# Optimization experiments

Hardware: AMD Instinct MI355X
Metric: run time of the kernel (lower is better)

## Reference

```python
import jax, jax.numpy as jnp
import numpy as np

B, NQ, NC, D, H = 4, 4096, 4096, 1024, 16
HD = D // H
LN_EPS = 1e-5


def _layernorm(x, g, b):
    mu = jnp.mean(x, axis=-1, keepdims=True)
    var = jnp.var(x, axis=-1, keepdims=True)
    return (x - mu) * jax.lax.rsqrt(var + LN_EPS) * g + b


def _kernel(x):
    # elu(x) + 1  (strictly positive feature map)
    return jax.nn.elu(x) + 1.0


def setup_inputs() -> dict:
    key = jax.random.key(0)
    ks = jax.random.split(key, 12)
    s = 1.0 / np.sqrt(D)
    return {
        "query": jax.random.normal(ks[0], (B, NQ, D), jnp.float32),
        "context": jax.random.normal(ks[1], (B, NC, D), jnp.float32),
        "q_w": jax.random.uniform(ks[2], (D, D), jnp.float32, -s, s),
        "q_b": jnp.zeros((D,), jnp.float32),
        "k_w": jax.random.uniform(ks[3], (D, D), jnp.float32, -s, s),
        "k_b": jnp.zeros((D,), jnp.float32),
        "v_w": jax.random.uniform(ks[4], (D, D), jnp.float32, -s, s),
        "v_b": jnp.zeros((D,), jnp.float32),
        "o_w": jax.random.uniform(ks[5], (D, D), jnp.float32, -s, s),
        "o_b": jnp.zeros((D,), jnp.float32),
        "lnq_g": jnp.ones((D,), jnp.float32),
        "lnq_b": jnp.zeros((D,), jnp.float32),
        "lnkv_g": jnp.ones((D,), jnp.float32),
        "lnkv_b": jnp.zeros((D,), jnp.float32),
    }


def reference(query, context, q_w, q_b, k_w, k_b, v_w, v_b, o_w, o_b,
              lnq_g, lnq_b, lnkv_g, lnkv_b):
    residual = query
    q = _layernorm(query, lnq_g, lnq_b)
    c = _layernorm(context, lnkv_g, lnkv_b)

    # torch Linear: y = x @ W.T + b ; reshape to (B, H, N, Hd)
    Q = (q @ q_w.T + q_b).reshape(B, NQ, H, HD).transpose(0, 2, 1, 3)
    K = (c @ k_w.T + k_b).reshape(B, NC, H, HD).transpose(0, 2, 1, 3)
    V = (c @ v_w.T + v_b).reshape(B, NC, H, HD).transpose(0, 2, 1, 3)

    Q = _kernel(Q)
    K = _kernel(K)

    # KV: (B, H, Hd, Hd) outer-product accumulation over context length
    KV = jnp.einsum("bhnd,bhne->bhde", K, V)
    K_sum = K.sum(axis=2)                              # (B, H, Hd)
    Z = jnp.einsum("bhqd,bhd->bhq", Q, K_sum)          # (B, H, Nq)
    Z = jnp.maximum(Z, 1e-6)

    out = jnp.einsum("bhqd,bhde->bhqe", Q, KV) / Z[..., None]
    out = out.transpose(0, 2, 1, 3).reshape(B, NQ, D)
    return residual + (out @ o_w.T + o_b)
```

## Files before the change

### kernel.cpp

```cpp
#include <hip/hip_runtime.h>

#define DEV __device__ __forceinline__

typedef __attribute__((ext_vector_type(8))) short short8;
typedef __attribute__((ext_vector_type(4))) short short4v;
typedef __attribute__((ext_vector_type(4))) float f32x4;

DEV float bf2f(unsigned short u) { return __uint_as_float(((unsigned int)u) << 16); }
DEV unsigned short f2bf(float f) {
    unsigned int u = __float_as_uint(f);
    u += 0x7FFFu + ((u >> 16) & 1u);
    return (unsigned short)(u >> 16);
}

DEV float elu1(float v) { return v > 0.0f ? v + 1.0f : __expf(v); }

DEV void gload_lds16(const void* g, void* l) {
    __builtin_amdgcn_global_load_lds(
        (__attribute__((address_space(1))) unsigned int*)(g),
        (__attribute__((address_space(3))) unsigned int*)(l),
        16, 0, 0);
}

#define NROW 16384
#define DDIM 1024

__global__ __launch_bounds__(256) void ln_kernel(
    const float* __restrict__ query, const float* __restrict__ context,
    const float* __restrict__ lnq_g, const float* __restrict__ lnq_b,
    const float* __restrict__ lnk_g, const float* __restrict__ lnk_b,
    unsigned short* __restrict__ qln, unsigned short* __restrict__ cln)
{
    const int row = blockIdx.x;
    const bool isq = row < NROW;
    const int r = isq ? row : row - NROW;
    const float* src = (isq ? query : context) + (size_t)r * DDIM;
    const float* g   = isq ? lnq_g : lnk_g;
    const float* bb  = isq ? lnq_b : lnk_b;
    unsigned short* dst = (isq ? qln : cln) + (size_t)r * DDIM;

    const int tid = threadIdx.x;
    f32x4 x = *(const f32x4*)(src + tid * 4);
    float s  = x[0] + x[1] + x[2] + x[3];
    float sq = x[0]*x[0] + x[1]*x[1] + x[2]*x[2] + x[3]*x[3];
#pragma unroll
    for (int off = 32; off; off >>= 1) {
        s  += __shfl_xor(s, off);
        sq += __shfl_xor(sq, off);
    }
    __shared__ float red[8];
    const int lane = tid & 63, w = tid >> 6;
    if (lane == 0) { red[w] = s; red[4 + w] = sq; }
    __syncthreads();
    s  = red[0] + red[1] + red[2] + red[3];
    sq = red[4] + red[5] + red[6] + red[7];
    const float mu  = s * (1.0f / DDIM);
    const float var = sq * (1.0f / DDIM) - mu * mu;
    const float rstd = rsqrtf(var + 1e-5f);

    f32x4 gv = *(const f32x4*)(g + tid * 4);
    f32x4 bv = *(const f32x4*)(bb + tid * 4);
    short4v o;
#pragma unroll
    for (int j = 0; j < 4; ++j)
        o[j] = (short)f2bf((x[j] - mu) * rstd * gv[j] + bv[j]);
    *(short4v*)(dst + tid * 4) = o;
}

__global__ __launch_bounds__(256) void conv_w(
    const float* __restrict__ a, const float* __restrict__ b,
    const float* __restrict__ c, const float* __restrict__ d,
    unsigned short* __restrict__ out)
{
    const int i = blockIdx.x * 256 + threadIdx.x;
    const int mat = i >> 18;
    const int idx = (i & 262143) * 4;
    const float* src = mat == 0 ? a : mat == 1 ? b : mat == 2 ? c : d;
    f32x4 v = *(const f32x4*)(src + idx);
    short4v o;
#pragma unroll
    for (int j = 0; j < 4; ++j) o[j] = (short)f2bf(v[j]);
    *(short4v*)(out + (size_t)mat * 1048576 + idx) = o;
}

template <typename EPI>
DEV void gemm128(unsigned short* __restrict__ sA,
                 unsigned short* __restrict__ sB,
                 const unsigned short* __restrict__ Ap,
                 const unsigned short* __restrict__ Bp,
                 int m0, int n0, EPI epi)
{
    const int tid = threadIdx.x;
    const int lane = tid & 63, w = tid >> 6;
    const int wr = w >> 1, wc = w & 1;
    const int lr = lane & 15, lg = lane >> 4;

    const int srow = tid >> 3;
    const int cswz = (tid & 7) ^ (srow & 7);
    const unsigned short* gA0 = Ap + (size_t)(m0 + srow) * 1024 + cswz * 8;
    const unsigned short* gB0 = Bp + (size_t)(n0 + srow) * 1024 + cswz * 8;
    unsigned short* dA = sA + tid * 8;
    unsigned short* dB = sB + tid * 8;

    const int sw0 = ((0 + lg) ^ (lr & 7)) * 8;
    const int sw1 = ((4 + lg) ^ (lr & 7)) * 8;

    f32x4 acc[4][4];
#pragma unroll
    for (int i = 0; i < 4; ++i)
#pragma unroll
        for (int j = 0; j < 4; ++j)
#pragma unroll
            for (int e = 0; e < 4; ++e) acc[i][j][e] = 0.0f;

#define STG8(T)                                                               \
    {                                                                         \
        const int ko = (T) * 64;                                              \
        _Pragma("unroll")                                                     \
        for (int j = 0; j < 4; ++j) {                                         \
            gload_lds16(gA0 + ko + (size_t)j * 32768, dA + j * 2048);         \
            gload_lds16(gB0 + ko + (size_t)j * 32768, dB + j * 2048);         \
        }                                                                     \
    }

    STG8(0);
    for (int t = 0; t < 16; ++t) {
        asm volatile("s_waitcnt vmcnt(0)" ::: "memory");
        __builtin_amdgcn_s_barrier();

        short8 af[4], bf[4];
#pragma unroll
        for (int mt = 0; mt < 4; ++mt)
            af[mt] = *(const short8*)&sA[(wr * 64 + mt * 16 + lr) * 64 + sw0];
#pragma unroll
        for (int nt = 0; nt < 4; ++nt)
            bf[nt] = *(const short8*)&sB[(wc * 64 + nt * 16 + lr) * 64 + sw0];
        __builtin_amdgcn_s_setprio(1);
#pragma unroll
        for (int mt = 0; mt < 4; ++mt)
#pragma unroll
            for (int nt = 0; nt < 4; ++nt)
                acc[mt][nt] = __builtin_amdgcn_mfma_f32_16x16x32_bf16(
                    af[mt], bf[nt], acc[mt][nt], 0, 0, 0);
        __builtin_amdgcn_s_setprio(0);

#pragma unroll
        for (int mt = 0; mt < 4; ++mt)
            af[mt] = *(const short8*)&sA[(wr * 64 + mt * 16 + lr) * 64 + sw1];
#pragma unroll
        for (int nt = 0; nt < 4; ++nt)
            bf[nt] = *(const short8*)&sB[(wc * 64 + nt * 16 + lr) * 64 + sw1];
        asm volatile("s_waitcnt lgkmcnt(0)" ::: "memory");
        __builtin_amdgcn_s_barrier();
        if (t < 15) STG8(t + 1);
        __builtin_amdgcn_s_setprio(1);
#pragma unroll
        for (int mt = 0; mt < 4; ++mt)
#pragma unroll
            for (int nt = 0; nt < 4; ++nt)
                acc[mt][nt] = __builtin_amdgcn_mfma_f32_16x16x32_bf16(
                    af[mt], bf[nt], acc[mt][nt], 0, 0, 0);
        __builtin_amdgcn_s_setprio(0);
    }
#undef STG8

#pragma unroll
    for (int mt = 0; mt < 4; ++mt)
#pragma unroll
        for (int nt = 0; nt < 4; ++nt) {
            const int col = n0 + wc * 64 + nt * 16 + lr;
#pragma unroll
            for (int i = 0; i < 4; ++i) {
                const int row = m0 + wr * 64 + mt * 16 + lg * 4 + i;
                epi(row, col, acc[mt][nt][i]);
            }
        }
}

__global__ __launch_bounds__(256, 4) void gemm_qkv(
    const unsigned short* __restrict__ QLN, const unsigned short* __restrict__ WQ,
    const unsigned short* __restrict__ CLN, const unsigned short* __restrict__ WKV,
    unsigned short* __restrict__ Qm, unsigned short* __restrict__ KVT,
    const float* __restrict__ q_b, const float* __restrict__ k_b,
    const float* __restrict__ v_b)
{
    __shared__ __attribute__((aligned(16))) unsigned short sA[128 * 64];
    __shared__ __attribute__((aligned(16))) unsigned short sB[128 * 64];

    const int bid = blockIdx.x;
    const int l = (bid & 7) * 384 + (bid >> 3);

    if (l < 1024) {
        const int m0 = (l >> 3) * 128, n0 = (l & 7) * 128;
        gemm128(sA, sB, QLN, WQ, m0, n0,
            [&](int row, int col, float v) {
                v = elu1(v + q_b[col]);
                Qm[(size_t)row * 1024 + col] = f2bf(v);
            });
    } else {
        const int r = l - 1024;
        const int m0 = (r & 15) * 128, n0 = (r >> 4) * 128;
        gemm128(sA, sB, WKV, CLN, m0, n0,
            [&](int row, int col, float v) {
                if (row < 1024) v = elu1(v + k_b[row]);
                else            v = v + v_b[row - 1024];
                KVT[(size_t)row * NROW + col] = f2bf(v);
            });
    }
}

__global__ __launch_bounds__(256, 4) void gemm_out(
    const unsigned short* __restrict__ A2, const unsigned short* __restrict__ WO,
    float* __restrict__ Out, const float* __restrict__ o_b,
    const float* __restrict__ resid)
{
    __shared__ __attribute__((aligned(16))) unsigned short sA[128 * 64];
    __shared__ __attribute__((aligned(16))) unsigned short sB[128 * 64];

    const int bid = blockIdx.x;
    const int l = (bid & 7) * 128 + (bid >> 3);
    const int m0 = (l >> 3) * 128, n0 = (l & 7) * 128;
    gemm128(sA, sB, A2, WO, m0, n0,
        [&](int row, int col, float v) {
            Out[(size_t)row * 1024 + col] =
                v + o_b[col] + resid[(size_t)row * 1024 + col];
        });
}

__global__ __launch_bounds__(256) void kv_kernel(
    const unsigned short* __restrict__ VT, const unsigned short* __restrict__ KT,
    float* __restrict__ KVTp, float* __restrict__ Ksump)
{
    const int bh = blockIdx.x, sp = blockIdx.y;
    const int b = bh >> 4, h = bh & 15;
    const int tid = threadIdx.x, lane = tid & 63, w = tid >> 6;
    const int lr = lane & 15, lg = lane >> 4;

    f32x4 acc[4][4];
#pragma unroll
    for (int i = 0; i < 4; ++i)
#pragma unroll
        for (int j = 0; j < 4; ++j)
#pragma unroll
            for (int e = 0; e < 4; ++e) acc[i][j][e] = 0.0f;
    float kp[4] = {0.0f, 0.0f, 0.0f, 0.0f};

    const size_t colbase = (size_t)b * 4096 + sp * 1024 + w * 256 + lg * 8;
    const unsigned short* va = VT + (size_t)(h * 64 + lr) * NROW + colbase;
    const unsigned short* ka = KT + (size_t)(h * 64 + lr) * NROW + colbase;

    for (int ks = 0; ks < 8; ++ks) {
        short8 af[4], bfv[4];
#pragma unroll
        for (int mt = 0; mt < 4; ++mt)
            af[mt] = *(const short8*)(va + (size_t)mt * 16 * NROW + ks * 32);
#pragma unroll
        for (int nt = 0; nt < 4; ++nt)
            bfv[nt] = *(const short8*)(ka + (size_t)nt * 16 * NROW + ks * 32);
#pragma unroll
        for (int mt = 0; mt < 4; ++mt)
#pragma unroll
            for (int nt = 0; nt < 4; ++nt)
                acc[mt][nt] = __builtin_amdgcn_mfma_f32_16x16x32_bf16(
                    af[mt], bfv[nt], acc[mt][nt], 0, 0, 0);
#pragma unroll
        for (int nt = 0; nt < 4; ++nt)
#pragma unroll
            for (int j = 0; j < 8; ++j)
                kp[nt] += bf2f((unsigned short)bfv[nt][j]);
    }

#pragma unroll
    for (int nt = 0; nt < 4; ++nt) {
        kp[nt] += __shfl_xor(kp[nt], 16);
        kp[nt] += __shfl_xor(kp[nt], 32);
    }
    __shared__ float kred[4][64];
    if (lane < 16) {
#pragma unroll
        for (int nt = 0; nt < 4; ++nt) kred[w][nt * 16 + lane] = kp[nt];
    }

    __shared__ float red4[4][4096];
#pragma unroll
    for (int mt = 0; mt < 4; ++mt)
#pragma unroll
        for (int nt = 0; nt < 4; ++nt)
#pragma unroll
            for (int i = 0; i < 4; ++i)
                red4[w][(mt * 16 + lg * 4 + i) * 64 + nt * 16 + lr] = acc[mt][nt][i];
    __syncthreads();
    float* out = KVTp + ((size_t)sp * 64 + bh) * 4096;
    for (int i = tid; i < 4096; i += 256)
        out[i] = red4[0][i] + red4[1][i] + red4[2][i] + red4[3][i];
    if (tid < 64)
        Ksump[((size_t)sp * 64 + bh) * 64 + tid] =
            kred[0][tid] + kred[1][tid] + kred[2][tid] + kred[3][tid];
}

__global__ __launch_bounds__(256) void z_kernel(
    const unsigned short* __restrict__ Q, const float* __restrict__ Ksump,
    float* __restrict__ invZ)
{
    const int gid = blockIdx.x * 256 + threadIdx.x;
    const int n = gid >> 4, h = gid & 15;
    const int b = n >> 12;
    const unsigned short* q = Q + (size_t)n * DDIM + h * 64;
    const float* k0 = Ksump + ((size_t)((b << 4) + h)) * 64;
    float z = 0.0f;
#pragma unroll
    for (int it = 0; it < 8; ++it) {
        short8 v = *(const short8*)(q + it * 8);
#pragma unroll
        for (int j = 0; j < 8; ++j) {
            const int d = it * 8 + j;
            const float ksv = k0[d] + k0[d + 4096] + k0[d + 8192] + k0[d + 12288];
            z += bf2f((unsigned short)v[j]) * ksv;
        }
    }
    invZ[gid] = 1.0f / fmaxf(z, 1e-6f);
}

__global__ __launch_bounds__(256) void a2_kernel(
    const unsigned short* __restrict__ Q, const float* __restrict__ KVTp,
    const float* __restrict__ invZ, unsigned short* __restrict__ A2)
{
    const int m0 = blockIdx.x * 128, h = blockIdx.y;
    const int b = m0 >> 12, bh = (b << 4) + h;
    const int tid = threadIdx.x, lane = tid & 63, w = tid >> 6;
    const int wr = w >> 1, wc = w & 1;
    const int lr = lane & 15, lg = lane >> 4;

    f32x4 acc[4][2];
#pragma unroll
    for (int i = 0; i < 4; ++i)
#pragma unroll
        for (int j = 0; j < 2; ++j)
#pragma unroll
            for (int e = 0; e < 4; ++e) acc[i][j][e] = 0.0f;

    const unsigned short* qa = Q + (size_t)(m0 + wr * 64 + lr) * DDIM + h * 64 + lg * 8;
    const float* kvb = KVTp + (size_t)bh * 4096 + (wc * 32 + lr) * 64 + lg * 8;

#pragma unroll
    for (int ks = 0; ks < 2; ++ks) {
        short8 af[4];
#pragma unroll
        for (int mt = 0; mt < 4; ++mt)
            af[mt] = *(const short8*)(qa + (size_t)mt * 16 * DDIM + ks * 32);
        short8 bfv[2];
#pragma unroll
        for (int nt = 0; nt < 2; ++nt) {
            const float* p = kvb + nt * 16 * 64 + ks * 32;
            short8 t;
#pragma unroll
            for (int j = 0; j < 8; ++j) {
                float v = p[j] + p[j + 262144] + p[j + 2 * 262144] + p[j + 3 * 262144];
                t[j] = (short)f2bf(v);
            }
            bfv[nt] = t;
        }
#pragma unroll
        for (int mt = 0; mt < 4; ++mt)
#pragma unroll
            for (int nt = 0; nt < 2; ++nt)
                acc[mt][nt] = __builtin_amdgcn_mfma_f32_16x16x32_bf16(
                    af[mt], bfv[nt], acc[mt][nt], 0, 0, 0);
    }

#pragma unroll
    for (int mt = 0; mt < 4; ++mt)
#pragma unroll
        for (int nt = 0; nt < 2; ++nt)
#pragma unroll
            for (int i = 0; i < 4; ++i) {
                const int row = m0 + wr * 64 + mt * 16 + lg * 4 + i;
                const int col = h * 64 + wc * 32 + nt * 16 + lr;
                const float v = acc[mt][nt][i] * invZ[row * 16 + h];
                A2[(size_t)row * DDIM + col] = f2bf(v);
            }
}

extern "C" void kernel_launch(void* const* d_in, const int* in_sizes, int n_in,
                              void* d_out, int out_size, void* d_ws, size_t ws_size,
                              hipStream_t stream)
{
    const float* query   = (const float*)d_in[0];
    const float* context = (const float*)d_in[1];
    const float* q_w = (const float*)d_in[2];
    const float* q_b = (const float*)d_in[3];
    const float* k_w = (const float*)d_in[4];
    const float* k_b = (const float*)d_in[5];
    const float* v_w = (const float*)d_in[6];
    const float* v_b = (const float*)d_in[7];
    const float* o_w = (const float*)d_in[8];
    const float* o_b = (const float*)d_in[9];
    const float* lnq_g = (const float*)d_in[10];
    const float* lnq_b = (const float*)d_in[11];
    const float* lnk_g = (const float*)d_in[12];
    const float* lnk_b = (const float*)d_in[13];

    char* ws = (char*)d_ws;
    unsigned short* WQ  = (unsigned short*)(ws);
    unsigned short* WKV = (unsigned short*)(ws + (2u << 20));
    unsigned short* WO  = (unsigned short*)(ws + (6u << 20));
    unsigned short* QLN = (unsigned short*)(ws + (8u << 20));
    unsigned short* CLN = (unsigned short*)(ws + (40u << 20));
    unsigned short* Qm  = (unsigned short*)(ws + (72u << 20));
    unsigned short* KT  = (unsigned short*)(ws + (104u << 20));
    unsigned short* VT  = (unsigned short*)(ws + (136u << 20));
    float* KVTp  = (float*)(ws + (168u << 20));
    float* Ksump = (float*)(ws + (172u << 20));
    float* invZ  = (float*)(ws + (173u << 20));
    unsigned short* A2 = QLN;

    conv_w<<<4096, 256, 0, stream>>>(q_w, k_w, v_w, o_w, WQ);
    ln_kernel<<<2 * NROW, 256, 0, stream>>>(query, context, lnq_g, lnq_b,
                                            lnk_g, lnk_b, QLN, CLN);
    gemm_qkv<<<3072, 256, 0, stream>>>(QLN, WQ, CLN, WKV, Qm, KT,
                                       q_b, k_b, v_b);
    kv_kernel<<<dim3(64, 4), 256, 0, stream>>>(VT, KT, KVTp, Ksump);
    z_kernel<<<1024, 256, 0, stream>>>(Qm, Ksump, invZ);
    a2_kernel<<<dim3(128, 16), 256, 0, stream>>>(Qm, KVTp, invZ, A2);
    gemm_out<<<1024, 256, 0, stream>>>(A2, WO, (float*)d_out, o_b, query);
}
```

Before: 315.7 us.

## Replace output GEMM with 256x256-tile, 8-wave double-buffered pipelined kernel

Swaps the 128x128 output projection GEMM for a 256x256 tile kernel run by 512 threads. It double-buffers LDS loads through global_load_lds, interleaves fragment reads with MFMA quadrants, and uses s_setprio and explicit waitcnt scheduling. The aim is to raise arithmetic intensity and overlap memory with compute. The cost is only 256 blocks for the whole GPU, which may leave CUs underused, plus 128KB of LDS per block and heavy register use.

After: 316.9 us. About the same (+0.4%).

```diff
diff --git a/kernel.cpp b/kernel.cpp
--- a/kernel.cpp
+++ b/kernel.cpp
@@ -209,22 +209,170 @@
     }
 }
 
-__global__ __launch_bounds__(256, 4) void gemm_out(
-    const unsigned short* __restrict__ A2, const unsigned short* __restrict__ WO,
-    float* __restrict__ Out, const float* __restrict__ o_b,
+__global__ __launch_bounds__(512, 2) void gemm_out256(
+    const unsigned short* __restrict__ A, const unsigned short* __restrict__ Bm,
+    float* __restrict__ Cout, const float* __restrict__ bias,
     const float* __restrict__ resid)
 {
-    __shared__ __attribute__((aligned(16))) unsigned short sA[128 * 64];
-    __shared__ __attribute__((aligned(16))) unsigned short sB[128 * 64];
+    __shared__ __attribute__((aligned(16))) unsigned short smem[65536];
+    unsigned short* sAb = smem;
+    unsigned short* sBb = smem + 32768;
 
     const int bid = blockIdx.x;
-    const int l = (bid & 7) * 128 + (bid >> 3);
-    const int m0 = (l >> 3) * 128, n0 = (l & 7) * 128;
-    gemm128(sA, sB, A2, WO, m0, n0,
-        [&](int row, int col, float v) {
-            Out[(size_t)row * 1024 + col] =
-                v + o_b[col] + resid[(size_t)row * 1024 + col];
-        });
+    const int l = (bid & 7) * 32 + (bid >> 3);
+    const int m0 = (l >> 2) * 256, n0 = (l & 3) * 256;
+
+    const int tid = threadIdx.x;
+    const int lane = tid & 63, w = tid >> 6;
+    const int wr = w >> 2, wc = w & 3;
+    const int lr = lane & 15, lg = lane >> 4;
+
+    const int srow = tid >> 3;
+    const int cswz = (tid & 7) ^ (srow & 7);
+    const unsigned short* gA0 = A  + (size_t)(m0 + srow) * 1024 + cswz * 8;
+    const unsigned short* gB0 = Bm + (size_t)(n0 + srow) * 1024 + cswz * 8;
+
+    const int sw0 = ((0 + lg) ^ (lr & 7)) * 8;
+    const int sw1 = ((4 + lg) ^ (lr & 7)) * 8;
+
+    f32x4 acc[8][4];
+#pragma unroll
+    for (int i = 0; i < 8; ++i)
+#pragma unroll
+        for (int j = 0; j < 4; ++j)
+#pragma unroll
+            for (int e = 0; e < 4; ++e) acc[i][j][e] = 0.0f;
+
+#define STG(GP, SP, T)                                                        \
+    {                                                                         \
+        const unsigned short* g = (GP) + (T) * 64;                            \
+        unsigned short* d = (SP) + ((T) & 1) * 16384 + tid * 8;               \
+        _Pragma("unroll")                                                     \
+        for (int L = 0; L < 4; ++L)                                           \
+            gload_lds16(g + (size_t)L * 65536, d + L * 4096);                 \
+    }
+
+    STG(gB0, sBb, 0); STG(gA0, sAb, 0); STG(gB0, sBb, 1); STG(gA0, sAb, 1);
+    asm volatile("s_waitcnt vmcnt(8)" ::: "memory");
+    __builtin_amdgcn_s_barrier();
+
+    short8 bvl[2][2];
+#pragma unroll
+    for (int nt = 0; nt < 2; ++nt) {
+        const int rb = (wc * 64 + nt * 16 + lr) * 64;
+        bvl[nt][0] = *(const short8*)&sBb[rb + sw0];
+        bvl[nt][1] = *(const short8*)&sBb[rb + sw1];
+    }
+
+    for (int t = 0; t < 16; ++t) {
+        const unsigned short* bA = sAb + (t & 1) * 16384;
+        const unsigned short* bB = sBb + (t & 1) * 16384;
+        const unsigned short* bBn = sBb + ((t + 1) & 1) * 16384;
+        short8 afl[4][2], afh[4][2], bvh[2][2], bvln[2][2];
+
+#pragma unroll
+        for (int mt = 0; mt < 4; ++mt) {
+            const int ra = (wr * 128 + mt * 16 + lr) * 64;
+            afl[mt][0] = *(const short8*)&bA[ra + sw0];
+            afl[mt][1] = *(const short8*)&bA[ra + sw1];
+        }
+#pragma unroll
+        for (int mt = 0; mt < 4; ++mt) {
+            const int ra = (wr * 128 + (mt + 4) * 16 + lr) * 64;
+            afh[mt][0] = *(const short8*)&bA[ra + sw0];
+            afh[mt][1] = *(const short8*)&bA[ra + sw1];
+        }
+        asm volatile("s_waitcnt lgkmcnt(8)" ::: "memory");
+        __builtin_amdgcn_s_setprio(1);
+#pragma unroll
+        for (int kk = 0; kk < 2; ++kk)
+#pragma unroll
+            for (int mt = 0; mt < 4; ++mt)
+#pragma unroll
+                for (int nt = 0; nt < 2; ++nt)
+                    acc[mt][nt] = __builtin_amdgcn_mfma_f32_16x16x32_bf16(
+                        afl[mt][kk], bvl[nt][kk], acc[mt][nt], 0, 0, 0);
+        __builtin_amdgcn_s_setprio(0);
+        __builtin_amdgcn_s_barrier();
+
+#pragma unroll
+        for (int nt = 0; nt < 2; ++nt) {
+            const int rb = (wc * 64 + (nt + 2) * 16 + lr) * 64;
+            bvh[nt][0] = *(const short8*)&bB[rb + sw0];
+            bvh[nt][1] = *(const short8*)&bB[rb + sw1];
+        }
+        asm volatile("s_waitcnt lgkmcnt(4)" ::: "memory");
+        __builtin_amdgcn_s_setprio(1);
+#pragma unroll
+        for (int kk = 0; kk < 2; ++kk)
+#pragma unroll
+            for (int mt = 0; mt < 4; ++mt)
+#pragma unroll
+                for (int nt = 0; nt < 2; ++nt)
+                    acc[mt + 4][nt] = __builtin_amdgcn_mfma_f32_16x16x32_bf16(
+                        afh[mt][kk], bvl[nt][kk], acc[mt + 4][nt], 0, 0, 0);
+        __builtin_amdgcn_s_setprio(0);
+        asm volatile("s_waitcnt vmcnt(0)" ::: "memory");
+        __builtin_amdgcn_s_barrier();
+
+        if (t < 15) {
+#pragma unroll
+            for (int nt = 0; nt < 2; ++nt) {
+                const int rb = (wc * 64 + nt * 16 + lr) * 64;
+                bvln[nt][0] = *(const short8*)&bBn[rb + sw0];
+                bvln[nt][1] = *(const short8*)&bBn[rb + sw1];
+            }
+        }
+        if (t + 2 < 16) STG(gA0, sAb, t + 2);
+        if (t < 15) asm volatile("s_waitcnt lgkmcnt(4)" ::: "memory");
+        else        asm volatile("s_waitcnt lgkmcnt(0)" ::: "memory");
+        __builtin_amdgcn_s_setprio(1);
+#pragma unroll
+        for (int kk = 0; kk < 2; ++kk)
+#pragma unroll
+            for (int mt = 0; mt < 4; ++mt)
+#pragma unroll
+                for (int nt = 0; nt < 2; ++nt)
+                    acc[mt + 4][nt + 2] = __builtin_amdgcn_mfma_f32_16x16x32_bf16(
+                        afh[mt][kk], bvh[nt][kk], acc[mt + 4][nt + 2], 0, 0, 0);
+        __builtin_amdgcn_s_setprio(0);
+        __builtin_amdgcn_s_barrier();
+
+        if (t + 2 < 16) STG(gB0, sBb, t + 2);
+        __builtin_amdgcn_s_setprio(1);
+#pragma unroll
+        for (int kk = 0; kk < 2; ++kk)
+#pragma unroll
+            for (int mt = 0; mt < 4; ++mt)
+#pragma unroll
+                for (int nt = 0; nt < 2; ++nt)
+                    acc[mt][nt + 2] = __builtin_amdgcn_mfma_f32_16x16x32_bf16(
+                        afl[mt][kk], bvh[nt][kk], acc[mt][nt + 2], 0, 0, 0);
+        __builtin_amdgcn_s_setprio(0);
+
+        if (t < 15) {
+#pragma unroll
+            for (int nt = 0; nt < 2; ++nt) {
+                bvl[nt][0] = bvln[nt][0];
+                bvl[nt][1] = bvln[nt][1];
+            }
+        }
+    }
+#undef STG
+
+#pragma unroll
+    for (int mt = 0; mt < 8; ++mt) {
+#pragma unroll
+        for (int nt = 0; nt < 4; ++nt) {
+            const int col = n0 + wc * 64 + nt * 16 + lr;
+#pragma unroll
+            for (int i = 0; i < 4; ++i) {
+                const int row = m0 + wr * 128 + mt * 16 + lg * 4 + i;
+                Cout[(size_t)row * 1024 + col] =
+                    acc[mt][nt][i] + bias[col] + resid[(size_t)row * 1024 + col];
+            }
+        }
+    }
 }
 
 __global__ __launch_bounds__(256) void kv_kernel(
@@ -422,5 +570,5 @@
     kv_kernel<<<dim3(64, 4), 256, 0, stream>>>(VT, KT, KVTp, Ksump);
     z_kernel<<<1024, 256, 0, stream>>>(Qm, Ksump, invZ);
     a2_kernel<<<dim3(128, 16), 256, 0, stream>>>(Qm, KVTp, invZ, A2);
-    gemm_out<<<1024, 256, 0, stream>>>(A2, WO, (float*)d_out, o_b, query);
-}
+    gemm_out256<<<256, 512, 0, stream>>>(A2, WO, (float*)d_out, o_b, query);
+}
```
